# Kernel optimization log

Hardware: AMD Instinct MI355X
Metric: run time of the kernel (lower is better)

The kernel has to match this reference:

```python
import jax, jax.numpy as jnp
import numpy as np


def _gcn_layer(x, W, b, src, dst, n_dst):
    """DGL GraphConv with norm='both': D_dst^{-1/2} A D_src^{-1/2} X W + b."""
    n_src = x.shape[0]
    ones = jnp.ones(src.shape[0], dtype=x.dtype)
    out_deg = jnp.clip(jax.ops.segment_sum(ones, src, num_segments=n_src), 1.0)
    in_deg = jnp.clip(jax.ops.segment_sum(ones, dst, num_segments=n_dst), 1.0)
    xn = x * (out_deg ** -0.5)[:, None]          # [n_src, F] source-side norm
    agg = jax.ops.segment_sum(xn[src], dst, num_segments=n_dst)  # sparse SpMM
    agg = agg * (in_deg ** -0.5)[:, None]        # dest-side norm
    return agg @ W + b


def setup_inputs() -> dict:
    key = jax.random.key(0)
    ks = jax.random.split(key, 9)
    N0, N1, N2 = 200000, 100000, 50000
    E1, E2 = 1600000, 800000
    F_in, F_hid, F_out = 128, 256, 128
    x = jax.random.normal(ks[0], (N0, F_in), dtype=jnp.float32)
    src1 = jax.random.randint(ks[1], (E1,), 0, N0, dtype=jnp.int32)
    dst1 = jax.random.randint(ks[2], (E1,), 0, N1, dtype=jnp.int32)
    src2 = jax.random.randint(ks[3], (E2,), 0, N1, dtype=jnp.int32)
    dst2 = jax.random.randint(ks[4], (E2,), 0, N2, dtype=jnp.int32)
    # Glorot-uniform weights like dgl GraphConv reset_parameters
    lim1 = (6.0 / (F_in + F_hid)) ** 0.5
    lim2 = (6.0 / (F_hid + F_out)) ** 0.5
    W1 = jax.random.uniform(ks[5], (F_in, F_hid), jnp.float32, -lim1, lim1)
    b1 = jnp.zeros((F_hid,), jnp.float32)
    W2 = jax.random.uniform(ks[6], (F_hid, F_out), jnp.float32, -lim2, lim2)
    b2 = jnp.zeros((F_out,), jnp.float32)
    return {"x": x, "W1": W1, "b1": b1, "W2": W2, "b2": b2,
            "src1": src1, "dst1": dst1, "src2": src2, "dst2": dst2,
            "n_dst1": N1, "n_dst2": N2}


def reference(x, W1, b1, W2, b2, src1, dst1, src2, dst2, n_dst1, n_dst2):
    h = jax.nn.relu(_gcn_layer(x, W1, b1, src1, dst1, n_dst1))
    out = jax.nn.relu(_gcn_layer(h, W2, b2, src2, dst2, n_dst2))
    return out
```

## Files before the change

kernel.cpp:

```cpp
#include <hip/hip_runtime.h>
#include <hip/hip_bf16.h>

#define F1 128
#define F2 256
#define F3 128
#define CAP 64

#define NB1D 391
#define NB2D 196
#define NB1S 782
#define NB2S 391
#define CAPD 4608
#define CAPS 2432
#define GD1 0
#define GD2 391
#define GS1 587
#define GS2 1369

#define YPAD 100096

typedef __attribute__((ext_vector_type(8))) short bf16x8;
typedef __attribute__((ext_vector_type(4))) float f32x4;
typedef __attribute__((ext_vector_type(4))) unsigned int u32x4;

__device__ inline float bf2f(unsigned short u) {
    return __uint_as_float(((unsigned int)u) << 16);
}
__device__ inline unsigned short f2bf(float f) {
    __hip_bfloat16 b = __float2bfloat16(f);
    return *reinterpret_cast<unsigned short*>(&b);
}
__device__ inline unsigned int pack2(float lo, float hi) {
    return ((unsigned int)f2bf(hi) << 16) | f2bf(lo);
}

#define ACC_ROW(u, c)                                   \
    acc[0] = fmaf(c, bf2f(u.x & 0xffff), acc[0]);       \
    acc[1] = fmaf(c, bf2f(u.x >> 16), acc[1]);          \
    acc[2] = fmaf(c, bf2f(u.y & 0xffff), acc[2]);       \
    acc[3] = fmaf(c, bf2f(u.y >> 16), acc[3]);          \
    acc[4] = fmaf(c, bf2f(u.z & 0xffff), acc[4]);       \
    acc[5] = fmaf(c, bf2f(u.z >> 16), acc[5]);          \
    acc[6] = fmaf(c, bf2f(u.w & 0xffff), acc[6]);       \
    acc[7] = fmaf(c, bf2f(u.w >> 16), acc[7]);

#define ACC_ROW_ADD(u)                          \
    acc[0] += bf2f(u.x & 0xffff);               \
    acc[1] += bf2f(u.x >> 16);                  \
    acc[2] += bf2f(u.y & 0xffff);               \
    acc[3] += bf2f(u.y >> 16);                  \
    acc[4] += bf2f(u.z & 0xffff);               \
    acc[5] += bf2f(u.z >> 16);                  \
    acc[6] += bf2f(u.w & 0xffff);               \
    acc[7] += bf2f(u.w >> 16);

__global__ __launch_bounds__(1024) void scatter_build(
    const int* __restrict__ src1, const int* __restrict__ dst1,
    const int* __restrict__ src2, const int* __restrict__ dst2,
    const float* __restrict__ x, const float* __restrict__ W1,
    const float* __restrict__ W2, int* __restrict__ gcnt,
    unsigned int* __restrict__ bkt_d1, unsigned int* __restrict__ bkt_d2,
    unsigned char* __restrict__ bkt_s1, unsigned char* __restrict__ bkt_s2,
    unsigned int* __restrict__ xn, unsigned short* __restrict__ Bp1,
    unsigned short* __restrict__ Bp2, int E1, int E2, int A1, int A2, int B3) {
    __shared__ int hist[800];
    __shared__ int scanA[800], scanB[800];
    __shared__ unsigned int stg[8192];
    __shared__ unsigned short bmap[8192];
    int b = blockIdx.x, t = threadIdx.x;

    if (b < A1 + A2) {
        const int L1 = (b < A1);
        const int* __restrict__ src = L1 ? src1 : src2;
        const int* __restrict__ dst = L1 ? dst1 : dst2;
        const int E = L1 ? E1 : E2;
        const int NBd = L1 ? NB1D : NB2D;
        const int NBs = L1 ? NB1S : NB2S;
        int* gd = gcnt + (L1 ? GD1 : GD2);
        int* gs = gcnt + (L1 ? GS1 : GS2);
        unsigned int* bd = L1 ? bkt_d1 : bkt_d2;
        unsigned char* bs = L1 ? bkt_s1 : bkt_s2;
        int e0 = (L1 ? b : b - A1) * 8192;
        int se[8], de[8];
#pragma unroll
        for (int k = 0; k < 8; ++k) {
            int e = e0 + k * 1024 + t;
            se[k] = -1;
            de[k] = -1;
            if (e < E) {
                se[k] = src[e];
                de[k] = dst[e];
            }
        }

        for (int i = t; i < NBd; i += 1024) hist[i] = 0;
        __syncthreads();
#pragma unroll
        for (int k = 0; k < 8; ++k)
            if (de[k] >= 0) atomicAdd(&hist[de[k] >> 8], 1);
        __syncthreads();
        {
            int* sa = scanA;
            int* sb = scanB;
            for (int i = t; i < NBd; i += 1024) sa[i] = hist[i];
            __syncthreads();
            for (int off = 1; off < NBd; off <<= 1) {
                for (int i = t; i < NBd; i += 1024) {
                    int v = sa[i];
                    if (i >= off) v += sa[i - off];
                    sb[i] = v;
                }
                __syncthreads();
                int* tp = sa; sa = sb; sb = tp;
            }
            for (int i = t; i < NBd; i += 1024) sb[i] = sa[i] - hist[i];
            __syncthreads();
#pragma unroll
            for (int k = 0; k < 8; ++k) {
                if (de[k] >= 0) {
                    int bk = de[k] >> 8;
                    int p = atomicAdd(&sb[bk], 1);
                    stg[p] = ((unsigned int)se[k] << 8) | (de[k] & 255);
                    bmap[p] = (unsigned short)bk;
                }
            }
            __syncthreads();
            for (int i = t; i < NBd; i += 1024) {
                int c = hist[i];
                int g = c ? atomicAdd(&gd[i], c) : 0;
                sb[i] = g - (sa[i] - c);
            }
            __syncthreads();
            int total = sa[NBd - 1];
            for (int i = t; i < total; i += 1024) {
                int bk = bmap[i];
                int gpos = sb[bk] + i;
                if (gpos < CAPD) bd[(size_t)bk * CAPD + gpos] = stg[i];
            }
        }
        __syncthreads();

        for (int i = t; i < NBs; i += 1024) hist[i] = 0;
        __syncthreads();
#pragma unroll
        for (int k = 0; k < 8; ++k)
            if (se[k] >= 0) atomicAdd(&hist[se[k] >> 8], 1);
        __syncthreads();
        {
            int* sa = scanA;
            int* sb = scanB;
            for (int i = t; i < NBs; i += 1024) sa[i] = hist[i];
            __syncthreads();
            for (int off = 1; off < NBs; off <<= 1) {
                for (int i = t; i < NBs; i += 1024) {
                    int v = sa[i];
                    if (i >= off) v += sa[i - off];
                    sb[i] = v;
                }
                __syncthreads();
                int* tp = sa; sa = sb; sb = tp;
            }
            for (int i = t; i < NBs; i += 1024) sb[i] = sa[i] - hist[i];
            __syncthreads();
#pragma unroll
            for (int k = 0; k < 8; ++k) {
                if (se[k] >= 0) {
                    int bk = se[k] >> 8;
                    int p = atomicAdd(&sb[bk], 1);
                    stg[p] = (unsigned int)(se[k] & 255);
                    bmap[p] = (unsigned short)bk;
                }
            }
            __syncthreads();
            for (int i = t; i < NBs; i += 1024) {
                int c = hist[i];
                int g = c ? atomicAdd(&gs[i], c) : 0;
                sb[i] = g - (sa[i] - c);
            }
            __syncthreads();
            int total = sa[NBs - 1];
            for (int i = t; i < total; i += 1024) {
                int bk = bmap[i];
                int gpos = sb[bk] + i;
                if (gpos < CAPS) bs[(size_t)bk * CAPS + gpos] = (unsigned char)stg[i];
            }
        }
    } else if (b < A1 + A2 + B3) {
        size_t tid = (size_t)(b - A1 - A2) * 1024 + t;
        const f32x4* xp = (const f32x4*)x;
        f32x4 a = __builtin_nontemporal_load(xp + tid * 2);
        f32x4 c = __builtin_nontemporal_load(xp + tid * 2 + 1);
        u32x4 o;
        o.x = pack2(a.x, a.y);
        o.y = pack2(a.z, a.w);
        o.z = pack2(c.x, c.y);
        o.w = pack2(c.z, c.w);
        ((u32x4*)xn)[tid] = o;
    } else {
        int w = b - (A1 + A2 + B3);
        int which = w >> 5;
        const float* W = which ? W2 : W1;
        unsigned short* out = which ? Bp2 : Bp1;
        int N = which ? F3 : F2;
        int idx = (w & 31) * 1024 + t;
        int k = idx / N, n = idx % N;
        unsigned short v = f2bf(W[idx]);
        int kt = k >> 5, q = (k >> 3) & 3, j = k & 7;
        int nt = n >> 4, lane = q * 16 + (n & 15);
        int NT = N >> 4;
        out[(((kt * NT + nt) * 64 + lane) << 3) + j] = v;
    }
}

__global__ __launch_bounds__(1024) void bucket_build(
    const int* __restrict__ gcnt,
    const unsigned int* __restrict__ bkt_d1, const unsigned int* __restrict__ bkt_d2,
    const unsigned char* __restrict__ bkt_s1, const unsigned char* __restrict__ bkt_s2,
    int* __restrict__ csr1, int* __restrict__ cnt_in1, float* __restrict__ rs_in1,
    int* __restrict__ csr2, int* __restrict__ cnt_in2, float* __restrict__ rs_in2,
    float* __restrict__ rs_out1, float* __restrict__ rs_out2) {
    __shared__ int hist[256];
    int b = blockIdx.x, t = threadIdx.x;
    if (t < 256) hist[t] = 0;
    __syncthreads();

    if (b < NB1D + NB2D) {
        const int L1 = (b < NB1D);
        int bb = L1 ? b : b - NB1D;
        const unsigned int* bkt = L1 ? bkt_d1 : bkt_d2;
        int* csr = L1 ? csr1 : csr2;
        int* cnt_in = L1 ? cnt_in1 : cnt_in2;
        float* rs_in = L1 ? rs_in1 : rs_in2;
        int Nd = L1 ? 100000 : 50000;
        int n = gcnt[(L1 ? GD1 : GD2) + bb];
        if (n > CAPD) n = CAPD;
        size_t base = (size_t)bb * CAPD;
        for (int i = t; i < n; i += 1024) {
            unsigned int v = bkt[base + i];
            int d = v & 255, s = (int)(v >> 8);
            int pos = atomicAdd(&hist[d], 1);
            if (pos < CAP) csr[((size_t)(bb * 256 + d)) * CAP + pos] = s;
        }
        __syncthreads();
        int node = bb * 256 + t;
        if (t < 256 && node < Nd) {
            int c = hist[t];
            cnt_in[node] = c < CAP ? c : CAP;
            rs_in[node] = rsqrtf((float)(c < 1 ? 1 : c));
        }
    } else {
        const int L1 = (b < NB1D + NB2D + NB1S);
        int bb = L1 ? b - (NB1D + NB2D) : b - (NB1D + NB2D + NB1S);
        const unsigned char* bkt = L1 ? bkt_s1 : bkt_s2;
        float* rs_out = L1 ? rs_out1 : rs_out2;
        int Ns = L1 ? 200000 : 100000;
        int n = gcnt[(L1 ? GS1 : GS2) + bb];
        if (n > CAPS) n = CAPS;
        size_t base = (size_t)bb * CAPS;
        for (int i = t; i < n; i += 1024) atomicAdd(&hist[bkt[base + i]], 1);
        __syncthreads();
        int node = bb * 256 + t;
        if (t < 256 && node < Ns) rs_out[node] = rsqrtf((float)(hist[t] < 1 ? 1 : hist[t]));
    }
}

__global__ __launch_bounds__(256) void agg128_kernel(
    const unsigned int* __restrict__ X, const int* __restrict__ csr,
    const int* __restrict__ cnt, const float* __restrict__ rs_src,
    unsigned int* __restrict__ out, int ndst) {
    int wave = (int)((blockIdx.x * blockDim.x + threadIdx.x) >> 6);
    int lane = threadIdx.x & 63;
    if (wave >= ndst) return;
    size_t base = (size_t)wave * CAP;
    int len = cnt[wave];
    int sl = 0;
    float clv = 0.f;
    if (lane < len) {
        sl = csr[base + lane];
        clv = rs_src[sl];
    }
    int eg = lane >> 4, fs = lane & 15;
    float acc[8];
#pragma unroll
    for (int i = 0; i < 8; ++i) acc[i] = 0.f;
    for (int j = 0; j < len; j += 16) {
        int jA = j + eg, jB = j + 4 + eg, jC = j + 8 + eg, jD = j + 12 + eg;
        int sA = __shfl(sl, jA);
        int sB = __shfl(sl, jB);
        int sC = __shfl(sl, jC);
        int sD = __shfl(sl, jD);
        float cA = __shfl(clv, jA);
        float cB = __shfl(clv, jB);
        float cC = __shfl(clv, jC);
        float cD = __shfl(clv, jD);
        u32x4 uA = *(const u32x4*)(X + (size_t)sA * 64 + (fs << 2));
        u32x4 uB = *(const u32x4*)(X + (size_t)sB * 64 + (fs << 2));
        u32x4 uC = *(const u32x4*)(X + (size_t)sC * 64 + (fs << 2));
        u32x4 uD = *(const u32x4*)(X + (size_t)sD * 64 + (fs << 2));
        ACC_ROW(uA, cA)
        ACC_ROW(uB, cB)
        ACC_ROW(uC, cC)
        ACC_ROW(uD, cD)
    }
#pragma unroll
    for (int i = 0; i < 8; ++i) {
        acc[i] += __shfl_xor(acc[i], 16);
        acc[i] += __shfl_xor(acc[i], 32);
    }
    if (eg == 0) {
        u32x4 o;
        o.x = pack2(acc[0], acc[1]);
        o.y = pack2(acc[2], acc[3]);
        o.z = pack2(acc[4], acc[5]);
        o.w = pack2(acc[6], acc[7]);
        *((u32x4*)(out + (size_t)wave * 64) + fs) = o;
    }
}

__global__ __launch_bounds__(512) void gemm12(
    const unsigned short* __restrict__ A,
    const unsigned short* __restrict__ Bp1,
    const unsigned short* __restrict__ Bp2,
    const float* __restrict__ rs1, const float* __restrict__ rs2,
    const float* __restrict__ bias1,
    unsigned short* __restrict__ Y, int M) {
    __shared__ unsigned short Bs[32768];
    __shared__ unsigned short tmp[128][264];
    int lane = threadIdx.x & 63, wid = threadIdx.x >> 6;
    int t = threadIdx.x;
    int row0 = blockIdx.x * 128 + wid * 16;
    int q = lane >> 4, col = lane & 15;

    u32x4 b2r[8];
#pragma unroll
    for (int i = 0; i < 8; ++i) {
        ((u32x4*)Bs)[i * 512 + t] = ((const u32x4*)Bp1)[i * 512 + t];
        b2r[i] = ((const u32x4*)Bp2)[i * 512 + t];
    }
    __syncthreads();

    int mload = row0 + col;
    if (mload > M - 1) mload = M - 1;
    const unsigned short* Arow = A + (size_t)mload * F1 + q * 8;
    f32x4 acc[16];
#pragma unroll
    for (int i = 0; i < 16; ++i) acc[i] = (f32x4){0.f, 0.f, 0.f, 0.f};
#pragma unroll
    for (int kt = 0; kt < 4; ++kt) {
        bf16x8 a = *(const bf16x8*)(Arow + kt * 32);
#pragma unroll
        for (int nt = 0; nt < 16; ++nt) {
            bf16x8 bfr = *(const bf16x8*)(Bs + (((kt * 16 + nt) * 64 + lane) << 3));
            acc[nt] = __builtin_amdgcn_mfma_f32_16x16x32_bf16(a, bfr, acc[nt], 0, 0, 0);
        }
    }
#pragma unroll
    for (int r = 0; r < 4; ++r) {
        int lrow = wid * 16 + q * 4 + r;
        int m = row0 + q * 4 + r;
        int mc = m < M ? m : M - 1;
        float s1 = rs1[mc], s2 = rs2[mc];
#pragma unroll
        for (int nt = 0; nt < 16; ++nt) {
            float v = fmaxf(fmaf(acc[nt][r], s1, bias1[nt * 16 + col]), 0.f) * s2;
            tmp[lrow][nt * 16 + col] = f2bf(v);
        }
    }
    __syncthreads();

#pragma unroll
    for (int i = 0; i < 8; ++i)
        ((u32x4*)Bs)[i * 512 + t] = b2r[i];
    __syncthreads();

    f32x4 acc2[8];
#pragma unroll
    for (int i = 0; i < 8; ++i) acc2[i] = (f32x4){0.f, 0.f, 0.f, 0.f};
    const unsigned short* trow = &tmp[wid * 16 + col][q * 8];
#pragma unroll
    for (int kt = 0; kt < 8; ++kt) {
        bf16x8 a = *(const bf16x8*)(trow + kt * 32);
#pragma unroll
        for (int nt = 0; nt < 8; ++nt) {
            bf16x8 bfr = *(const bf16x8*)(Bs + (((kt * 8 + nt) * 64 + lane) << 3));
            acc2[nt] = __builtin_amdgcn_mfma_f32_16x16x32_bf16(a, bfr, acc2[nt], 0, 0, 0);
        }
    }
#pragma unroll
    for (int r = 0; r < 4; ++r) {
        int m = row0 + q * 4 + r;
        int live = m < M;
#pragma unroll
        for (int nt = 0; nt < 8; ++nt)
            Y[(size_t)m * F3 + nt * 16 + col] = live ? f2bf(acc2[nt][r]) : (unsigned short)0;
    }
}

__global__ __launch_bounds__(256) void agg_final(
    const unsigned int* __restrict__ Yv, const int* __restrict__ csr,
    const int* __restrict__ cnt, const float* __restrict__ rs_dst,
    const float* __restrict__ b2, float* __restrict__ out, int ndst, int zrow) {
    int wave = (int)((blockIdx.x * blockDim.x + threadIdx.x) >> 6);
    int lane = threadIdx.x & 63;
    if (wave >= ndst) return;
    size_t base = (size_t)wave * CAP;
    int len = cnt[wave];
    int sl = zrow;
    if (lane < len) sl = csr[base + lane];
    int eg = lane >> 4, fs = lane & 15;
    float acc[8];
#pragma unroll
    for (int i = 0; i < 8; ++i) acc[i] = 0.f;
    for (int j = 0; j < len; j += 16) {
        int jA = j + eg, jB = j + 4 + eg, jC = j + 8 + eg, jD = j + 12 + eg;
        int sA = __shfl(sl, jA);
        int sB = __shfl(sl, jB);
        int sC = __shfl(sl, jC);
        int sD = __shfl(sl, jD);
        u32x4 uA = *(const u32x4*)(Yv + (size_t)sA * 64 + (fs << 2));
        u32x4 uB = *(const u32x4*)(Yv + (size_t)sB * 64 + (fs << 2));
        u32x4 uC = *(const u32x4*)(Yv + (size_t)sC * 64 + (fs << 2));
        u32x4 uD = *(const u32x4*)(Yv + (size_t)sD * 64 + (fs << 2));
        ACC_ROW_ADD(uA)
        ACC_ROW_ADD(uB)
        ACC_ROW_ADD(uC)
        ACC_ROW_ADD(uD)
    }
#pragma unroll
    for (int i = 0; i < 8; ++i) {
        acc[i] += __shfl_xor(acc[i], 16);
        acc[i] += __shfl_xor(acc[i], 32);
    }
    if (eg < 2) {
        float sc = rs_dst[wave];
        f32x4 bias = ((const f32x4*)b2)[(fs << 1) | eg];
        float v0 = eg ? acc[4] : acc[0];
        float v1 = eg ? acc[5] : acc[1];
        float v2 = eg ? acc[6] : acc[2];
        float v3 = eg ? acc[7] : acc[3];
        f32x4 o;
        o.x = fmaxf(fmaf(v0, sc, bias.x), 0.f);
        o.y = fmaxf(fmaf(v1, sc, bias.y), 0.f);
        o.z = fmaxf(fmaf(v2, sc, bias.z), 0.f);
        o.w = fmaxf(fmaf(v3, sc, bias.w), 0.f);
        __builtin_nontemporal_store(o, (f32x4*)out + (size_t)wave * 32 + (fs << 1) + eg);
    }
}

extern "C" void kernel_launch(void* const* d_in, const int* in_sizes, int n_in,
                              void* d_out, int out_size, void* d_ws, size_t ws_size,
                              hipStream_t stream) {
    const float* x  = (const float*)d_in[0];
    const float* W1 = (const float*)d_in[1];
    const float* b1 = (const float*)d_in[2];
    const float* W2 = (const float*)d_in[3];
    const float* b2 = (const float*)d_in[4];
    const int* src1 = (const int*)d_in[5];
    const int* dst1 = (const int*)d_in[6];
    const int* src2 = (const int*)d_in[7];
    const int* dst2 = (const int*)d_in[8];
    const int E1 = in_sizes[5], E2 = in_sizes[7];
    const int N0 = in_sizes[0] / F1;
    const int N1 = 100000, N2 = 50000;

    char* p = (char*)d_ws;
    int* gcnt = (int*)p; p += 2048 * 4;
    float* rs_out1 = (float*)p; p += (size_t)N0 * 4;
    float* rs_in1  = (float*)p; p += (size_t)N1 * 4;
    float* rs_out2 = (float*)p; p += (size_t)N1 * 4;
    float* rs_in2  = (float*)p; p += (size_t)N2 * 4;
    int* cnt_in1 = (int*)p; p += (size_t)N1 * 4;
    int* cnt_in2 = (int*)p; p += (size_t)N2 * 4;
    unsigned int* bkt_d1 = (unsigned int*)p; p += (size_t)NB1D * CAPD * 4;
    unsigned int* bkt_d2 = (unsigned int*)p; p += (size_t)NB2D * CAPD * 4;
    unsigned char* bkt_s1 = (unsigned char*)p; p += (size_t)NB1S * CAPS;
    unsigned char* bkt_s2 = (unsigned char*)p; p += (size_t)NB2S * CAPS;
    int* csr1 = (int*)p; p += (size_t)N1 * CAP * 4;
    int* csr2 = (int*)p; p += (size_t)N2 * CAP * 4;
    unsigned short* Bp1 = (unsigned short*)p; p += (size_t)F1 * F2 * 2;
    unsigned short* Bp2 = (unsigned short*)p; p += (size_t)F2 * F3 * 2;
    unsigned short* xn  = (unsigned short*)p; p += (size_t)N0 * F1 * 2;
    unsigned short* agg = (unsigned short*)p; p += (size_t)N1 * F1 * 2;
    unsigned short* y = xn;

    (void)hipMemsetAsync(gcnt, 0, 2048 * 4, stream);

    int A1 = (E1 + 8191) / 8192;
    int A2 = (E2 + 8191) / 8192;
    int B3 = N0 * F1 / 8 / 1024;
    scatter_build<<<A1 + A2 + B3 + 64, 1024, 0, stream>>>(
        src1, dst1, src2, dst2, x, W1, W2, gcnt,
        bkt_d1, bkt_d2, bkt_s1, bkt_s2,
        (unsigned int*)xn, Bp1, Bp2, E1, E2, A1, A2, B3);

    bucket_build<<<NB1D + NB2D + NB1S + NB2S, 1024, 0, stream>>>(
        gcnt, bkt_d1, bkt_d2, bkt_s1, bkt_s2,
        csr1, cnt_in1, rs_in1, csr2, cnt_in2, rs_in2, rs_out1, rs_out2);

    agg128_kernel<<<(N1 + 3) / 4, 256, 0, stream>>>((const unsigned int*)xn, csr1,
                                                    cnt_in1, rs_out1,
                                                    (unsigned int*)agg, N1);

    gemm12<<<(N1 + 127) / 128, 512, 0, stream>>>(agg, Bp1, Bp2, rs_in1, rs_out2, b1, y, N1);

    agg_final<<<(N2 + 3) / 4, 256, 0, stream>>>((const unsigned int*)y, csr2, cnt_in2,
                                                rs_in2, b2, (float*)d_out, N2, N1);
}
```

Before: 349.4 us.

## Compute out-degrees via global atomics and fold source norm into bf16 conversion

Adds a separate deg_pass kernel that counts source out-degrees with global atomics, replacing the source-side bucket scatter and histogram path in scatter_build and bucket_build. The source-side normalisation is then applied while x is converted to bf16, and for layer 2 it is computed in the GEMM epilogue straight from the degree counts. This lets the first aggregation do plain adds without per-edge coefficient loads and shuffles. Out-of-range lanes now read a zeroed padding row instead of using a zero coefficient. In exchange there is one more kernel launch, a larger memset, and global atomic contention on the degree arrays.

New measurement: 431.6 us. 1.24x slower.

```diff
diff --git a/kernel.cpp b/kernel.cpp
--- a/kernel.cpp
+++ b/kernel.cpp
@@ -8,14 +8,9 @@
 
 #define NB1D 391
 #define NB2D 196
-#define NB1S 782
-#define NB2S 391
 #define CAPD 4608
-#define CAPS 2432
 #define GD1 0
 #define GD2 391
-#define GS1 587
-#define GS2 1369
 
 #define YPAD 100096
 
@@ -33,16 +28,9 @@
 __device__ inline unsigned int pack2(float lo, float hi) {
     return ((unsigned int)f2bf(hi) << 16) | f2bf(lo);
 }
-
-#define ACC_ROW(u, c)                                   \
-    acc[0] = fmaf(c, bf2f(u.x & 0xffff), acc[0]);       \
-    acc[1] = fmaf(c, bf2f(u.x >> 16), acc[1]);          \
-    acc[2] = fmaf(c, bf2f(u.y & 0xffff), acc[2]);       \
-    acc[3] = fmaf(c, bf2f(u.y >> 16), acc[3]);          \
-    acc[4] = fmaf(c, bf2f(u.z & 0xffff), acc[4]);       \
-    acc[5] = fmaf(c, bf2f(u.z >> 16), acc[5]);          \
-    acc[6] = fmaf(c, bf2f(u.w & 0xffff), acc[6]);       \
-    acc[7] = fmaf(c, bf2f(u.w >> 16), acc[7]);
+__device__ inline float rsdeg(int c) {
+    return rsqrtf((float)(c < 1 ? 1 : c));
+}
 
 #define ACC_ROW_ADD(u)                          \
     acc[0] += bf2f(u.x & 0xffff);               \
@@ -54,17 +42,39 @@
     acc[6] += bf2f(u.w & 0xffff);               \
     acc[7] += bf2f(u.w >> 16);
 
+__global__ __launch_bounds__(1024) void deg_pass(
+    const int* __restrict__ src1, const int* __restrict__ src2,
+    int* __restrict__ od1, int* __restrict__ od2, int E1, int E2, int A1) {
+    int b = blockIdx.x, t = threadIdx.x;
+    if (b < A1) {
+        int e0 = b * 8192;
+#pragma unroll
+        for (int k = 0; k < 8; ++k) {
+            int e = e0 + k * 1024 + t;
+            if (e < E1) atomicAdd(&od1[src1[e]], 1);
+        }
+    } else {
+        int e0 = (b - A1) * 8192;
+#pragma unroll
+        for (int k = 0; k < 8; ++k) {
+            int e = e0 + k * 1024 + t;
+            if (e < E2) atomicAdd(&od2[src2[e]], 1);
+        }
+    }
+}
+
 __global__ __launch_bounds__(1024) void scatter_build(
     const int* __restrict__ src1, const int* __restrict__ dst1,
     const int* __restrict__ src2, const int* __restrict__ dst2,
     const float* __restrict__ x, const float* __restrict__ W1,
     const float* __restrict__ W2, int* __restrict__ gcnt,
+    const int* __restrict__ outdeg1,
     unsigned int* __restrict__ bkt_d1, unsigned int* __restrict__ bkt_d2,
-    unsigned char* __restrict__ bkt_s1, unsigned char* __restrict__ bkt_s2,
     unsigned int* __restrict__ xn, unsigned short* __restrict__ Bp1,
-    unsigned short* __restrict__ Bp2, int E1, int E2, int A1, int A2, int B3) {
-    __shared__ int hist[800];
-    __shared__ int scanA[800], scanB[800];
+    unsigned short* __restrict__ Bp2, int E1, int E2, int A1, int A2, int B3,
+    int N0) {
+    __shared__ int hist[400];
+    __shared__ int scanA[400], scanB[400];
     __shared__ unsigned int stg[8192];
     __shared__ unsigned short bmap[8192];
     int b = blockIdx.x, t = threadIdx.x;
@@ -75,11 +85,8 @@
         const int* __restrict__ dst = L1 ? dst1 : dst2;
         const int E = L1 ? E1 : E2;
         const int NBd = L1 ? NB1D : NB2D;
-        const int NBs = L1 ? NB1S : NB2S;
         int* gd = gcnt + (L1 ? GD1 : GD2);
-        int* gs = gcnt + (L1 ? GS1 : GS2);
         unsigned int* bd = L1 ? bkt_d1 : bkt_d2;
-        unsigned char* bs = L1 ? bkt_s1 : bkt_s2;
         int e0 = (L1 ? b : b - A1) * 8192;
         int se[8], de[8];
 #pragma unroll
@@ -99,104 +106,57 @@
         for (int k = 0; k < 8; ++k)
             if (de[k] >= 0) atomicAdd(&hist[de[k] >> 8], 1);
         __syncthreads();
-        {
-            int* sa = scanA;
-            int* sb = scanB;
-            for (int i = t; i < NBd; i += 1024) sa[i] = hist[i];
-            __syncthreads();
-            for (int off = 1; off < NBd; off <<= 1) {
-                for (int i = t; i < NBd; i += 1024) {
-                    int v = sa[i];
-                    if (i >= off) v += sa[i - off];
-                    sb[i] = v;
-                }
-                __syncthreads();
-                int* tp = sa; sa = sb; sb = tp;
-            }
-            for (int i = t; i < NBd; i += 1024) sb[i] = sa[i] - hist[i];
-            __syncthreads();
-#pragma unroll
-            for (int k = 0; k < 8; ++k) {
-                if (de[k] >= 0) {
-                    int bk = de[k] >> 8;
-                    int p = atomicAdd(&sb[bk], 1);
-                    stg[p] = ((unsigned int)se[k] << 8) | (de[k] & 255);
-                    bmap[p] = (unsigned short)bk;
-                }
+        int* sa = scanA;
+        int* sb = scanB;
+        for (int i = t; i < NBd; i += 1024) sa[i] = hist[i];
+        __syncthreads();
+        for (int off = 1; off < NBd; off <<= 1) {
+            for (int i = t; i < NBd; i += 1024) {
+                int v = sa[i];
+                if (i >= off) v += sa[i - off];
+                sb[i] = v;
             }
             __syncthreads();
-            for (int i = t; i < NBd; i += 1024) {
-                int c = hist[i];
-                int g = c ? atomicAdd(&gd[i], c) : 0;
-                sb[i] = g - (sa[i] - c);
+            int* tp = sa; sa = sb; sb = tp;
+        }
+        for (int i = t; i < NBd; i += 1024) sb[i] = sa[i] - hist[i];
+        __syncthreads();
+#pragma unroll
+        for (int k = 0; k < 8; ++k) {
+            if (de[k] >= 0) {
+                int bk = de[k] >> 8;
+                int p = atomicAdd(&sb[bk], 1);
+                stg[p] = ((unsigned int)se[k] << 8) | (de[k] & 255);
+                bmap[p] = (unsigned short)bk;
             }
-            __syncthreads();
-            int total = sa[NBd - 1];
-            for (int i = t; i < total; i += 1024) {
-                int bk = bmap[i];
-                int gpos = sb[bk] + i;
-                if (gpos < CAPD) bd[(size_t)bk * CAPD + gpos] = stg[i];
-            }
-        }
-        __syncthreads();
-
-        for (int i = t; i < NBs; i += 1024) hist[i] = 0;
-        __syncthreads();
-#pragma unroll
-        for (int k = 0; k < 8; ++k)
-            if (se[k] >= 0) atomicAdd(&hist[se[k] >> 8], 1);
-        __syncthreads();
-        {
-            int* sa = scanA;
-            int* sb = scanB;
-            for (int i = t; i < NBs; i += 1024) sa[i] = hist[i];
-            __syncthreads();
-            for (int off = 1; off < NBs; off <<= 1) {
-                for (int i = t; i < NBs; i += 1024) {
-                    int v = sa[i];
-                    if (i >= off) v += sa[i - off];
-                    sb[i] = v;
-                }
-                __syncthreads();
-                int* tp = sa; sa = sb; sb = tp;
-            }
-            for (int i = t; i < NBs; i += 1024) sb[i] = sa[i] - hist[i];
-            __syncthreads();
-#pragma unroll
-            for (int k = 0; k < 8; ++k) {
-                if (se[k] >= 0) {
-                    int bk = se[k] >> 8;
-                    int p = atomicAdd(&sb[bk], 1);
-                    stg[p] = (unsigned int)(se[k] & 255);
-                    bmap[p] = (unsigned short)bk;
-                }
-            }
-            __syncthreads();
-            for (int i = t; i < NBs; i += 1024) {
-                int c = hist[i];
-                int g = c ? atomicAdd(&gs[i], c) : 0;
-                sb[i] = g - (sa[i] - c);
-            }
-            __syncthreads();
-            int total = sa[NBs - 1];
-            for (int i = t; i < total; i += 1024) {
-                int bk = bmap[i];
-                int gpos = sb[bk] + i;
-                if (gpos < CAPS) bs[(size_t)bk * CAPS + gpos] = (unsigned char)stg[i];
-            }
+        }
+        __syncthreads();
+        for (int i = t; i < NBd; i += 1024) {
+            int c = hist[i];
+            int g = c ? atomicAdd(&gd[i], c) : 0;
+            sb[i] = g - (sa[i] - c);
+        }
+        __syncthreads();
+        int total = sa[NBd - 1];
+        for (int i = t; i < total; i += 1024) {
+            int bk = bmap[i];
+            int gpos = sb[bk] + i;
+            if (gpos < CAPD) bd[(size_t)bk * CAPD + gpos] = stg[i];
         }
     } else if (b < A1 + A2 + B3) {
         size_t tid = (size_t)(b - A1 - A2) * 1024 + t;
+        int row = (int)(tid >> 4);
+        float s = rsdeg(outdeg1[row]);
         const f32x4* xp = (const f32x4*)x;
         f32x4 a = __builtin_nontemporal_load(xp + tid * 2);
         f32x4 c = __builtin_nontemporal_load(xp + tid * 2 + 1);
         u32x4 o;
-        o.x = pack2(a.x, a.y);
-        o.y = pack2(a.z, a.w);
-        o.z = pack2(c.x, c.y);
-        o.w = pack2(c.z, c.w);
+        o.x = pack2(a.x * s, a.y * s);
+        o.y = pack2(a.z * s, a.w * s);
+        o.z = pack2(c.x * s, c.y * s);
+        o.w = pack2(c.z * s, c.w * s);
         ((u32x4*)xn)[tid] = o;
-    } else {
+    } else if (b < A1 + A2 + B3 + 64) {
         int w = b - (A1 + A2 + B3);
         int which = w >> 5;
         const float* W = which ? W2 : W1;
@@ -209,76 +169,57 @@
         int nt = n >> 4, lane = q * 16 + (n & 15);
         int NT = N >> 4;
         out[(((kt * NT + nt) * 64 + lane) << 3) + j] = v;
+    } else {
+        if (t < 64) xn[(size_t)N0 * 64 + t] = 0u;
     }
 }
 
 __global__ __launch_bounds__(1024) void bucket_build(
     const int* __restrict__ gcnt,
     const unsigned int* __restrict__ bkt_d1, const unsigned int* __restrict__ bkt_d2,
-    const unsigned char* __restrict__ bkt_s1, const unsigned char* __restrict__ bkt_s2,
     int* __restrict__ csr1, int* __restrict__ cnt_in1, float* __restrict__ rs_in1,
-    int* __restrict__ csr2, int* __restrict__ cnt_in2, float* __restrict__ rs_in2,
-    float* __restrict__ rs_out1, float* __restrict__ rs_out2) {
+    int* __restrict__ csr2, int* __restrict__ cnt_in2, float* __restrict__ rs_in2) {
     __shared__ int hist[256];
     int b = blockIdx.x, t = threadIdx.x;
     if (t < 256) hist[t] = 0;
     __syncthreads();
 
-    if (b < NB1D + NB2D) {
-        const int L1 = (b < NB1D);
-        int bb = L1 ? b : b - NB1D;
-        const unsigned int* bkt = L1 ? bkt_d1 : bkt_d2;
-        int* csr = L1 ? csr1 : csr2;
-        int* cnt_in = L1 ? cnt_in1 : cnt_in2;
-        float* rs_in = L1 ? rs_in1 : rs_in2;
-        int Nd = L1 ? 100000 : 50000;
-        int n = gcnt[(L1 ? GD1 : GD2) + bb];
-        if (n > CAPD) n = CAPD;
-        size_t base = (size_t)bb * CAPD;
-        for (int i = t; i < n; i += 1024) {
-            unsigned int v = bkt[base + i];
-            int d = v & 255, s = (int)(v >> 8);
-            int pos = atomicAdd(&hist[d], 1);
-            if (pos < CAP) csr[((size_t)(bb * 256 + d)) * CAP + pos] = s;
-        }
-        __syncthreads();
-        int node = bb * 256 + t;
-        if (t < 256 && node < Nd) {
-            int c = hist[t];
-            cnt_in[node] = c < CAP ? c : CAP;
-            rs_in[node] = rsqrtf((float)(c < 1 ? 1 : c));
-        }
-    } else {
-        const int L1 = (b < NB1D + NB2D + NB1S);
-        int bb = L1 ? b - (NB1D + NB2D) : b - (NB1D + NB2D + NB1S);
-        const unsigned char* bkt = L1 ? bkt_s1 : bkt_s2;
-        float* rs_out = L1 ? rs_out1 : rs_out2;
-        int Ns = L1 ? 200000 : 100000;
-        int n = gcnt[(L1 ? GS1 : GS2) + bb];
-        if (n > CAPS) n = CAPS;
-        size_t base = (size_t)bb * CAPS;
-        for (int i = t; i < n; i += 1024) atomicAdd(&hist[bkt[base + i]], 1);
-        __syncthreads();
-        int node = bb * 256 + t;
-        if (t < 256 && node < Ns) rs_out[node] = rsqrtf((float)(hist[t] < 1 ? 1 : hist[t]));
+    const int L1 = (b < NB1D);
+    int bb = L1 ? b : b - NB1D;
+    const unsigned int* bkt = L1 ? bkt_d1 : bkt_d2;
+    int* csr = L1 ? csr1 : csr2;
+    int* cnt_in = L1 ? cnt_in1 : cnt_in2;
+    float* rs_in = L1 ? rs_in1 : rs_in2;
+    int Nd = L1 ? 100000 : 50000;
+    int n = gcnt[(L1 ? GD1 : GD2) + bb];
+    if (n > CAPD) n = CAPD;
+    size_t base = (size_t)bb * CAPD;
+    for (int i = t; i < n; i += 1024) {
+        unsigned int v = bkt[base + i];
+        int d = v & 255, s = (int)(v >> 8);
+        int pos = atomicAdd(&hist[d], 1);
+        if (pos < CAP) csr[((size_t)(bb * 256 + d)) * CAP + pos] = s;
+    }
+    __syncthreads();
+    int node = bb * 256 + t;
+    if (t < 256 && node < Nd) {
+        int c = hist[t];
+        cnt_in[node] = c < CAP ? c : CAP;
+        rs_in[node] = rsqrtf((float)(c < 1 ? 1 : c));
     }
 }
 
 __global__ __launch_bounds__(256) void agg128_kernel(
     const unsigned int* __restrict__ X, const int* __restrict__ csr,
-    const int* __restrict__ cnt, const float* __restrict__ rs_src,
-    unsigned int* __restrict__ out, int ndst) {
+    const int* __restrict__ cnt, unsigned int* __restrict__ out, int ndst,
+    int zrow) {
     int wave = (int)((blockIdx.x * blockDim.x + threadIdx.x) >> 6);
     int lane = threadIdx.x & 63;
     if (wave >= ndst) return;
     size_t base = (size_t)wave * CAP;
     int len = cnt[wave];
-    int sl = 0;
-    float clv = 0.f;
-    if (lane < len) {
-        sl = csr[base + lane];
-        clv = rs_src[sl];
-    }
+    int sl = zrow;
+    if (lane < len) sl = csr[base + lane];
     int eg = lane >> 4, fs = lane & 15;
     float acc[8];
 #pragma unroll
@@ -289,18 +230,14 @@
         int sB = __shfl(sl, jB);
         int sC = __shfl(sl, jC);
         int sD = __shfl(sl, jD);
-        float cA = __shfl(clv, jA);
-        float cB = __shfl(clv, jB);
-        float cC = __shfl(clv, jC);
-        float cD = __shfl(clv, jD);
         u32x4 uA = *(const u32x4*)(X + (size_t)sA * 64 + (fs << 2));
         u32x4 uB = *(const u32x4*)(X + (size_t)sB * 64 + (fs << 2));
         u32x4 uC = *(const u32x4*)(X + (size_t)sC * 64 + (fs << 2));
         u32x4 uD = *(const u32x4*)(X + (size_t)sD * 64 + (fs << 2));
-        ACC_ROW(uA, cA)
-        ACC_ROW(uB, cB)
-        ACC_ROW(uC, cC)
-        ACC_ROW(uD, cD)
+        ACC_ROW_ADD(uA)
+        ACC_ROW_ADD(uB)
+        ACC_ROW_ADD(uC)
+        ACC_ROW_ADD(uD)
     }
 #pragma unroll
     for (int i = 0; i < 8; ++i) {
@@ -321,7 +258,7 @@
     const unsigned short* __restrict__ A,
     const unsigned short* __restrict__ Bp1,
     const unsigned short* __restrict__ Bp2,
-    const float* __restrict__ rs1, const float* __restrict__ rs2,
+    const float* __restrict__ rs1, const int* __restrict__ od2,
     const float* __restrict__ bias1,
     unsigned short* __restrict__ Y, int M) {
     __shared__ unsigned short Bs[32768];
@@ -359,7 +296,7 @@
         int lrow = wid * 16 + q * 4 + r;
         int m = row0 + q * 4 + r;
         int mc = m < M ? m : M - 1;
-        float s1 = rs1[mc], s2 = rs2[mc];
+        float s1 = rs1[mc], s2 = rsdeg(od2[mc]);
 #pragma unroll
         for (int nt = 0; nt < 16; ++nt) {
             float v = fmaxf(fmaf(acc[nt][r], s1, bias1[nt * 16 + col]), 0.f) * s2;
@@ -464,44 +401,44 @@
     const int N1 = 100000, N2 = 50000;
 
     char* p = (char*)d_ws;
-    int* gcnt = (int*)p; p += 2048 * 4;
-    float* rs_out1 = (float*)p; p += (size_t)N0 * 4;
+    int* gcnt    = (int*)p; p += 1024 * 4;
+    int* outdeg1 = (int*)p; p += (size_t)N0 * 4;
+    int* outdeg2 = (int*)p; p += (size_t)N1 * 4;
+    size_t zero_bytes = 1024 * 4 + (size_t)N0 * 4 + (size_t)N1 * 4;
     float* rs_in1  = (float*)p; p += (size_t)N1 * 4;
-    float* rs_out2 = (float*)p; p += (size_t)N1 * 4;
     float* rs_in2  = (float*)p; p += (size_t)N2 * 4;
     int* cnt_in1 = (int*)p; p += (size_t)N1 * 4;
     int* cnt_in2 = (int*)p; p += (size_t)N2 * 4;
     unsigned int* bkt_d1 = (unsigned int*)p; p += (size_t)NB1D * CAPD * 4;
     unsigned int* bkt_d2 = (unsigned int*)p; p += (size_t)NB2D * CAPD * 4;
-    unsigned char* bkt_s1 = (unsigned char*)p; p += (size_t)NB1S * CAPS;
-    unsigned char* bkt_s2 = (unsigned char*)p; p += (size_t)NB2S * CAPS;
     int* csr1 = (int*)p; p += (size_t)N1 * CAP * 4;
     int* csr2 = (int*)p; p += (size_t)N2 * CAP * 4;
     unsigned short* Bp1 = (unsigned short*)p; p += (size_t)F1 * F2 * 2;
     unsigned short* Bp2 = (unsigned short*)p; p += (size_t)F2 * F3 * 2;
-    unsigned short* xn  = (unsigned short*)p; p += (size_t)N0 * F1 * 2;
+    unsigned short* xn  = (unsigned short*)p; p += (size_t)(N0 + 8) * F1 * 2;
     unsigned short* agg = (unsigned short*)p; p += (size_t)N1 * F1 * 2;
     unsigned short* y = xn;
 
-    (void)hipMemsetAsync(gcnt, 0, 2048 * 4, stream);
+    (void)hipMemsetAsync(gcnt, 0, zero_bytes, stream);
 
     int A1 = (E1 + 8191) / 8192;
     int A2 = (E2 + 8191) / 8192;
     int B3 = N0 * F1 / 8 / 1024;
-    scatter_build<<<A1 + A2 + B3 + 64, 1024, 0, stream>>>(
-        src1, dst1, src2, dst2, x, W1, W2, gcnt,
-        bkt_d1, bkt_d2, bkt_s1, bkt_s2,
-        (unsigned int*)xn, Bp1, Bp2, E1, E2, A1, A2, B3);
-
-    bucket_build<<<NB1D + NB2D + NB1S + NB2S, 1024, 0, stream>>>(
-        gcnt, bkt_d1, bkt_d2, bkt_s1, bkt_s2,
-        csr1, cnt_in1, rs_in1, csr2, cnt_in2, rs_in2, rs_out1, rs_out2);
+
+    deg_pass<<<A1 + A2, 1024, 0, stream>>>(src1, src2, outdeg1, outdeg2, E1, E2, A1);
+
+    scatter_build<<<A1 + A2 + B3 + 65, 1024, 0, stream>>>(
+        src1, dst1, src2, dst2, x, W1, W2, gcnt, outdeg1,
+        bkt_d1, bkt_d2, (unsigned int*)xn, Bp1, Bp2, E1, E2, A1, A2, B3, N0);
+
+    bucket_build<<<NB1D + NB2D, 1024, 0, stream>>>(
+        gcnt, bkt_d1, bkt_d2, csr1, cnt_in1, rs_in1, csr2, cnt_in2, rs_in2);
 
     agg128_kernel<<<(N1 + 3) / 4, 256, 0, stream>>>((const unsigned int*)xn, csr1,
-                                                    cnt_in1, rs_out1,
-                                                    (unsigned int*)agg, N1);
-
-    gemm12<<<(N1 + 127) / 128, 512, 0, stream>>>(agg, Bp1, Bp2, rs_in1, rs_out2, b1, y, N1);
+                                                    cnt_in1, (unsigned int*)agg,
+                                                    N1, N0);
+
+    gemm12<<<(N1 + 127) / 128, 512, 0, stream>>>(agg, Bp1, Bp2, rs_in1, outdeg2, b1, y, N1);
 
     agg_final<<<(N2 + 3) / 4, 256, 0, stream>>>((const unsigned int*)y, csr2, cnt_in2,
                                                 rs_in2, b2, (float*)d_out, N2, N1);
```
